# Kernel optimization log

Measured on AMD Instinct MI355X. Metric: run time of the kernel, lower is better.

## Reference

```python
import jax, jax.numpy as jnp
import numpy as np

N = 50000          # nodes
E = 800000         # edges (before self-loops)
IN_CH = 16
HID = 32
HEADS = 4
NEG_SLOPE = 0.2    # PyG GATConv default leaky_relu slope


def add_self_loops(edge_index, n):
    loops = jnp.arange(n, dtype=edge_index.dtype)
    return jnp.concatenate([edge_index, jnp.stack([loops, loops])], axis=1)


def gat_layer(x, edge_index, W, a_src, a_dst, bias, heads, out_ch, concat):
    """PyG-style GATConv: gather -> attention logits -> segment softmax over dst -> scatter."""
    n = x.shape[0]
    h = (x @ W).reshape(n, heads, out_ch)            # [N, H, C]
    src, dst = edge_index[0], edge_index[1]          # messages flow src -> dst
    alpha_src = (h * a_src).sum(-1)                  # [N, H]
    alpha_dst = (h * a_dst).sum(-1)                  # [N, H]
    e = jax.nn.leaky_relu(alpha_src[src] + alpha_dst[dst], NEG_SLOPE)  # [Etot, H]
    # numerically stable segment softmax over incoming edges of each dst node
    e_max = jax.ops.segment_max(e, dst, num_segments=n)
    e_exp = jnp.exp(e - e_max[dst])
    denom = jax.ops.segment_sum(e_exp, dst, num_segments=n)
    alpha = e_exp / (denom[dst] + 1e-16)             # [Etot, H]
    out = jax.ops.segment_sum(h[src] * alpha[..., None], dst, num_segments=n)  # [N, H, C]
    out = out.reshape(n, heads * out_ch) if concat else out.mean(axis=1)
    return out + bias


def setup_inputs() -> dict:
    key = jax.random.key(0)
    ks = jax.random.split(key, 10)
    x = jax.random.normal(ks[0], (N, IN_CH), dtype=jnp.float32)
    edge_index = jax.random.randint(ks[1], (2, E), 0, N, dtype=jnp.int64)
    s = 0.1
    W1 = jax.random.normal(ks[2], (IN_CH, HEADS * HID), dtype=jnp.float32) * s
    a_src1 = jax.random.normal(ks[3], (1, HEADS, HID), dtype=jnp.float32) * s
    a_dst1 = jax.random.normal(ks[4], (1, HEADS, HID), dtype=jnp.float32) * s
    b1 = jnp.zeros((HEADS * HID,), dtype=jnp.float32)
    W2 = jax.random.normal(ks[5], (HEADS * HID, 2), dtype=jnp.float32) * s
    a_src2 = jax.random.normal(ks[6], (1, 1, 2), dtype=jnp.float32) * s
    a_dst2 = jax.random.normal(ks[7], (1, 1, 2), dtype=jnp.float32) * s
    b2 = jnp.zeros((2,), dtype=jnp.float32)
    return {"x": x, "edge_index": edge_index,
            "W1": W1, "a_src1": a_src1, "a_dst1": a_dst1, "b1": b1,
            "W2": W2, "a_src2": a_src2, "a_dst2": a_dst2, "b2": b2}


def reference(x, edge_index, W1, a_src1, a_dst1, b1, W2, a_src2, a_dst2, b2):
    ei = add_self_loops(edge_index, x.shape[0])
    h = gat_layer(x, ei, W1, a_src1, a_dst1, b1, HEADS, HID, concat=True)
    h = jax.nn.relu(h)
    out = gat_layer(h, ei, W2, a_src2, a_dst2, b2, 1, 2, concat=False)
    return out
```

## Files before the change

### kernel.cpp

```cpp
#include <hip/hip_runtime.h>
#include <hip/hip_bf16.h>

#define N_NODES 50000
#define N_EDGES 800000
#define ETOT    (N_EDGES + N_NODES)
#define STRIDE  64
#define IN_CH   16
#define HID     32
#define HEADS   4
#define C1      (HEADS * HID)
#define NEG     0.2f
#define NSLICE  8
#define SLICE_N (N_NODES / NSLICE)

#define DEG_BLOCKS  ((ETOT / 4 + 255) / 256)
#define FILL_BLOCKS (NSLICE * DEG_BLOCKS)
#define NGROUPS     (N_NODES / 4)
#define H1_BLOCKS   2048

typedef unsigned short u16;
typedef unsigned int   u32;

__device__ __forceinline__ float bf2f(u16 b) {
    return __uint_as_float(((u32)b) << 16);
}

__device__ __forceinline__ u16 f2bf(float f) {
    __hip_bfloat16 hb = __float2bfloat16(f);
    return *(u16*)&hb;
}

__device__ __forceinline__ int clampn(int v) {
    return v < 0 ? 0 : (v >= N_NODES ? N_NODES - 1 : v);
}

__device__ __forceinline__ int eidx(const int* ei, int e, int i64, int which) {
    int v = i64 ? ei[2 * (which * N_EDGES + e)] : ei[which * N_EDGES + e];
    return clampn(v);
}

__device__ __forceinline__ float cvt(const void* src, int i, int bf) {
    return bf ? bf2f(((const u16*)src)[i]) : ((const float*)src)[i];
}

__device__ __forceinline__ int probe_bf_wave(const u16* xb) {
    int l = threadIdx.x & 63;
    int my = 0;
#pragma unroll
    for (int k = 0; k < 4; k++) {
        float f = bf2f(xb[l * 4 + k]);
        float a = fabsf(f);
        if (f == 0.0f || (a > 9.5e-7f && a < 1.05e6f)) my++;
    }
#pragma unroll
    for (int m = 32; m; m >>= 1) my += __shfl_xor(my, m);
    return __builtin_amdgcn_readfirstlane(my >= 224 ? 1 : 0);
}

__device__ __forceinline__ int probe_i64_wave(const int* ei32) {
    int l = threadIdx.x & 63;
    int nz = (l < 32 && ei32[2 * l + 1] != 0) ? 1 : 0;
#pragma unroll
    for (int m = 32; m; m >>= 1) nz += __shfl_xor(nz, m);
    return __builtin_amdgcn_readfirstlane(nz == 0 ? 1 : 0);
}

__device__ __forceinline__ void dev_degfill(const int* __restrict__ ei,
                                            int* __restrict__ degs,
                                            u16* __restrict__ csr, int blk) {
    int slice = blk & (NSLICE - 1);
    int chunk = blk >> 3;
    int i64 = probe_i64_wave(ei);
    int e0 = (chunk * 256 + (int)threadIdx.x) * 4;
    if (e0 >= ETOT) return;
    int lo = slice * SLICE_N, hi = lo + SLICE_N;
    int s[4], d[4];
#pragma unroll
    for (int j = 0; j < 4; j++) {
        int e = e0 + j;
        if (e < N_EDGES) { s[j] = eidx(ei, e, i64, 0); d[j] = eidx(ei, e, i64, 1); }
        else             { s[j] = d[j] = e - N_EDGES; }
    }
#pragma unroll
    for (int j = 0; j < 4; j++) {
        if (d[j] >= lo && d[j] < hi) {
            u32 r = (u32)atomicAdd(&degs[d[j]], 1) + 1u;
            if (r < STRIDE) csr[(size_t)d[j] * STRIDE + r] = (u16)s[j];
        }
    }
}

__device__ __forceinline__ void dev_h1(const void* __restrict__ x,
                                       const void* __restrict__ W1,
                                       const void* __restrict__ a_s,
                                       const void* __restrict__ a_d,
                                       float* __restrict__ as1,
                                       float* __restrict__ ad1, int blk) {
    int bf = probe_bf_wave((const u16*)x);
    int w = threadIdx.x >> 6, l = threadIdx.x & 63;

    float wa[IN_CH], wb[IN_CH];
    if (bf) {
        const u32* w32 = (const u32*)W1;
#pragma unroll
        for (int k = 0; k < IN_CH; k++) {
            u32 v = w32[k * 64 + l];
            wa[k] = bf2f((u16)(v & 0xFFFF));
            wb[k] = bf2f((u16)(v >> 16));
        }
    } else {
        const float2* w64 = (const float2*)W1;
#pragma unroll
        for (int k = 0; k < IN_CH; k++) {
            float2 v = w64[k * 64 + l];
            wa[k] = v.x; wb[k] = v.y;
        }
    }
    float asa, asb, ada, adb;
    if (bf) {
        u32 vs = ((const u32*)a_s)[l], vd = ((const u32*)a_d)[l];
        asa = bf2f((u16)(vs & 0xFFFF)); asb = bf2f((u16)(vs >> 16));
        ada = bf2f((u16)(vd & 0xFFFF)); adb = bf2f((u16)(vd >> 16));
    } else {
        float2 vs = ((const float2*)a_s)[l], vd = ((const float2*)a_d)[l];
        asa = vs.x; asb = vs.y; ada = vd.x; adb = vd.y;
    }

    for (int g = blk; g < NGROUPS; g += H1_BLOCKS) {
        int n = g * 4 + w;
        float xr[IN_CH];
        if (bf) {
            const uint4* xp = (const uint4*)((const u16*)x + (size_t)n * IN_CH);
            uint4 q0 = xp[0], q1 = xp[1];
            u32 qq[8] = {q0.x, q0.y, q0.z, q0.w, q1.x, q1.y, q1.z, q1.w};
#pragma unroll
            for (int k = 0; k < 8; k++) {
                xr[2 * k]     = bf2f((u16)(qq[k] & 0xFFFF));
                xr[2 * k + 1] = bf2f((u16)(qq[k] >> 16));
            }
        } else {
            const float4* xp = (const float4*)((const float*)x + (size_t)n * IN_CH);
#pragma unroll
            for (int k = 0; k < 4; k++) {
                float4 q = xp[k];
                xr[4 * k] = q.x; xr[4 * k + 1] = q.y;
                xr[4 * k + 2] = q.z; xr[4 * k + 3] = q.w;
            }
        }
        float acc0 = 0.f, acc1 = 0.f;
#pragma unroll
        for (int k = 0; k < IN_CH; k++) {
            acc0 += xr[k] * wa[k];
            acc1 += xr[k] * wb[k];
        }
        float ps = acc0 * asa + acc1 * asb;
        float pd = acc0 * ada + acc1 * adb;
#pragma unroll
        for (int m = 8; m; m >>= 1) { ps += __shfl_xor(ps, m); pd += __shfl_xor(pd, m); }
        if ((l & 15) == 0) {
            int hd = l >> 4;
            as1[n * 4 + hd] = ps;
            ad1[n * 4 + hd] = pd;
        }
    }
}

__launch_bounds__(256)
__global__ void k_fill_h1(const void* __restrict__ x, const int* __restrict__ ei,
                          const void* __restrict__ W1, const void* __restrict__ a_s,
                          const void* __restrict__ a_d,
                          int* __restrict__ degs, u16* __restrict__ csr,
                          float* __restrict__ as1, float* __restrict__ ad1) {
    if (blockIdx.x < FILL_BLOCKS) { dev_degfill(ei, degs, csr, blockIdx.x); return; }
    dev_h1(x, W1, a_s, a_d, as1, ad1, blockIdx.x - FILL_BLOCKS);
}

__launch_bounds__(256)
__global__ void k_gather1(const void* __restrict__ x,
                          const int* __restrict__ degs, const u16* __restrict__ csr,
                          const float* __restrict__ as1, const float* __restrict__ ad1,
                          const void* __restrict__ W1,
                          const void* __restrict__ b1, const void* __restrict__ W2,
                          const void* __restrict__ a2s, const void* __restrict__ a2d,
                          float* __restrict__ h2, float* __restrict__ as2,
                          float* __restrict__ ad2) {
    __shared__ float xs[4][64][17];
    __shared__ float ws[4][64][4];
    int wv = threadIdx.x >> 6;
    int n  = blockIdx.x * 4 + wv;
    int l  = threadIdx.x & 63;
    int h  = l >> 4;
    int k  = l & 15;
    int g16 = l & 48;

    const u16* row = csr + (size_t)n * STRIDE;
    int se   = (int)row[l];
    int degv = degs[n];
    float4 d4 = ((const float4*)ad1)[n];

    int bf = probe_bf_wave((const u16*)x);

    int deg = degv + 1;
    deg = deg > STRIDE ? STRIDE : deg;
    int live = (l < deg);
    int sidx = (live && se < N_NODES) ? se : 0;

    if (live) {
        float4 a4 = ((const float4*)as1)[sidx];
        float xr[IN_CH];
        if (bf) {
            const uint4* xp = (const uint4*)((const u16*)x + (size_t)sidx * IN_CH);
            uint4 q0 = xp[0], q1 = xp[1];
            u32 qq[8] = {q0.x, q0.y, q0.z, q0.w, q1.x, q1.y, q1.z, q1.w};
#pragma unroll
            for (int kk = 0; kk < 8; kk++) {
                xr[2 * kk]     = bf2f((u16)(qq[kk] & 0xFFFF));
                xr[2 * kk + 1] = bf2f((u16)(qq[kk] >> 16));
            }
        } else {
            const float4* xp = (const float4*)((const float*)x + (size_t)sidx * IN_CH);
#pragma unroll
            for (int kk = 0; kk < 4; kk++) {
                float4 q = xp[kk];
                xr[4 * kk] = q.x; xr[4 * kk + 1] = q.y;
                xr[4 * kk + 2] = q.z; xr[4 * kk + 3] = q.w;
            }
        }
        float t0 = a4.x + d4.x; t0 = t0 > 0.f ? t0 : NEG * t0;
        float t1 = a4.y + d4.y; t1 = t1 > 0.f ? t1 : NEG * t1;
        float t2 = a4.z + d4.z; t2 = t2 > 0.f ? t2 : NEG * t2;
        float t3 = a4.w + d4.w; t3 = t3 > 0.f ? t3 : NEG * t3;
#pragma unroll
        for (int kk = 0; kk < IN_CH; kk++) xs[wv][l][kk] = xr[kk];
        ws[wv][l][0] = __expf(t0); ws[wv][l][1] = __expf(t1);
        ws[wv][l][2] = __expf(t2); ws[wv][l][3] = __expf(t3);
    }

    float wa[IN_CH], wb[IN_CH];
    if (bf) {
        const u32* w32 = (const u32*)W1;
#pragma unroll
        for (int kk = 0; kk < IN_CH; kk++) {
            u32 v = w32[kk * 64 + l];
            wa[kk] = bf2f((u16)(v & 0xFFFF));
            wb[kk] = bf2f((u16)(v >> 16));
        }
    } else {
        const float2* w64 = (const float2*)W1;
#pragma unroll
        for (int kk = 0; kk < IN_CH; kk++) {
            float2 v = w64[kk * 64 + l];
            wa[kk] = v.x; wb[kk] = v.y;
        }
    }
    float b1v0 = cvt(b1, 2 * l, bf),     b1v1 = cvt(b1, 2 * l + 1, bf);
    float w2a  = cvt(W2, 4 * l, bf),     w2b  = cvt(W2, 4 * l + 1, bf);
    float w2c  = cvt(W2, 4 * l + 2, bf), w2d  = cvt(W2, 4 * l + 3, bf);
    float a2s0 = cvt(a2s, 0, bf), a2s1 = cvt(a2s, 1, bf);
    float a2d0 = cvt(a2d, 0, bf), a2d1 = cvt(a2d, 1, bf);

    __syncthreads();

    float acc = 0.f, sws = 0.f;
#pragma unroll 4
    for (int j = 0; j < deg; j++) {
        float w = ws[wv][j][h];
        acc += w * xs[wv][j][k];
        sws += w;
    }
    float aggn = acc * (1.0f / sws);

    float o0 = 0.f, o1 = 0.f;
#pragma unroll
    for (int kk = 0; kk < IN_CH; kk++) {
        float a = __shfl(aggn, g16 + kk);
        o0 += a * wa[kk];
        o1 += a * wb[kk];
    }
    float v0 = o0 + b1v0;
    float v1 = o1 + b1v1;
    v0 = v0 > 0.f ? v0 : 0.f;
    v1 = v1 > 0.f ? v1 : 0.f;
    float p0 = v0 * w2a + v1 * w2c;
    float p1 = v0 * w2b + v1 * w2d;
#pragma unroll
    for (int d = 32; d; d >>= 1) { p0 += __shfl_down(p0, d); p1 += __shfl_down(p1, d); }
    if (l == 0) {
        h2[n * 2] = p0; h2[n * 2 + 1] = p1;
        as2[n] = p0 * a2s0 + p1 * a2s1;
        ad2[n] = p0 * a2d0 + p1 * a2d1;
    }
}

__launch_bounds__(256)
__global__ void k_gather2(const void* __restrict__ x,
                          const int* __restrict__ degs, const u16* __restrict__ csr,
                          const float* __restrict__ h2, const float* __restrict__ as2,
                          const float* __restrict__ ad2, const void* __restrict__ b2,
                          void* __restrict__ out) {
    int n = blockIdx.x * 16 + (threadIdx.x >> 4);
    int g = threadIdx.x & 15;
    int degv = degs[n];
    float adv = ad2[n];
    const u16* row = csr + (size_t)n * STRIDE;
    int bf = probe_bf_wave((const u16*)x);
    float a0 = 0.f, a1 = 0.f, sw = 0.f;
    int deg = degv + 1;
    deg = deg > STRIDE ? STRIDE : deg;
    for (int k = g; k < deg; k += 16) {
        int s = (int)row[k];
        float lg = as2[s] + adv;
        lg = lg > 0.f ? lg : NEG * lg;
        float w = __expf(lg);
        float2 hv = ((const float2*)h2)[s];
        a0 += w * hv.x;
        a1 += w * hv.y;
        sw += w;
    }
#pragma unroll
    for (int m = 8; m; m >>= 1) {
        a0 += __shfl_xor(a0, m); a1 += __shfl_xor(a1, m); sw += __shfl_xor(sw, m);
    }
    if (g == 0) {
        float inv = 1.0f / sw;
        float o0 = a0 * inv + cvt(b2, 0, bf);
        float o1 = a1 * inv + cvt(b2, 1, bf);
        if (bf) {
            ((u32*)out)[n] = (u32)f2bf(o0) | ((u32)f2bf(o1) << 16);
        } else {
            ((float2*)out)[n] = make_float2(o0, o1);
        }
    }
}

extern "C" void kernel_launch(void* const* d_in, const int* in_sizes, int n_in,
                              void* d_out, int out_size, void* d_ws, size_t ws_size,
                              hipStream_t stream) {
    const void* x    = d_in[0];
    const int*  ei   = (const int*)d_in[1];
    const void* W1   = d_in[2];
    const void* a_s1 = d_in[3];
    const void* a_d1 = d_in[4];
    const void* b1   = d_in[5];
    const void* W2   = d_in[6];
    const void* a_s2 = d_in[7];
    const void* a_d2 = d_in[8];
    const void* b2   = d_in[9];

    char* p = (char*)d_ws;
    int*   degs = (int*)p;     p += ((size_t)N_NODES * 4 + 255) & ~255;
    u16*   csr  = (u16*)p;     p += (size_t)N_NODES * STRIDE * 2;
    float* as1  = (float*)p;   p += (size_t)N_NODES * HEADS * 4;
    float* ad1  = (float*)p;   p += (size_t)N_NODES * HEADS * 4;
    float* h2   = (float*)p;   p += (size_t)N_NODES * 2 * 4;
    float* as2  = (float*)p;   p += (size_t)N_NODES * 4;
    float* ad2  = (float*)p;   p += (size_t)N_NODES * 4;

    hipMemsetAsync(degs, 0xFF, (size_t)N_NODES * 4, stream);

    k_fill_h1<<<FILL_BLOCKS + H1_BLOCKS, 256, 0, stream>>>(
        x, ei, W1, a_s1, a_d1, degs, csr, as1, ad1);
    k_gather1<<<N_NODES / 4, 256, 0, stream>>>(
        x, degs, csr, as1, ad1, W1, b1, W2, a_s2, a_d2, h2, as2, ad2);
    k_gather2<<<N_NODES / 16, 256, 0, stream>>>(
        x, degs, csr, h2, as2, ad2, b2, d_out);
}
```

Measured before the change: 206.7 us.

## Process two nodes per wave in gather1 and cache dtype probe flag

```diff
diff --git a/kernel.cpp b/kernel.cpp
--- a/kernel.cpp
+++ b/kernel.cpp
@@ -65,6 +65,27 @@
     return __builtin_amdgcn_readfirstlane(nz == 0 ? 1 : 0);
 }
 
+__device__ __forceinline__ void load_xrow(float* xr, const void* x, int sidx, int bf) {
+    if (bf) {
+        const uint4* xp = (const uint4*)((const u16*)x + (size_t)sidx * IN_CH);
+        uint4 q0 = xp[0], q1 = xp[1];
+        u32 qq[8] = {q0.x, q0.y, q0.z, q0.w, q1.x, q1.y, q1.z, q1.w};
+#pragma unroll
+        for (int kk = 0; kk < 8; kk++) {
+            xr[2 * kk]     = bf2f((u16)(qq[kk] & 0xFFFF));
+            xr[2 * kk + 1] = bf2f((u16)(qq[kk] >> 16));
+        }
+    } else {
+        const float4* xp = (const float4*)((const float*)x + (size_t)sidx * IN_CH);
+#pragma unroll
+        for (int kk = 0; kk < 4; kk++) {
+            float4 q = xp[kk];
+            xr[4 * kk] = q.x; xr[4 * kk + 1] = q.y;
+            xr[4 * kk + 2] = q.z; xr[4 * kk + 3] = q.w;
+        }
+    }
+}
+
 __device__ __forceinline__ void dev_degfill(const int* __restrict__ ei,
                                             int* __restrict__ degs,
                                             u16* __restrict__ csr, int blk) {
@@ -95,8 +116,10 @@
                                        const void* __restrict__ a_s,
                                        const void* __restrict__ a_d,
                                        float* __restrict__ as1,
-                                       float* __restrict__ ad1, int blk) {
+                                       float* __restrict__ ad1,
+                                       u32* __restrict__ flags, int blk) {
     int bf = probe_bf_wave((const u16*)x);
+    if (blk == 0 && threadIdx.x == 0) flags[0] = (u32)bf;
     int w = threadIdx.x >> 6, l = threadIdx.x & 63;
 
     float wa[IN_CH], wb[IN_CH];
@@ -129,24 +152,7 @@
     for (int g = blk; g < NGROUPS; g += H1_BLOCKS) {
         int n = g * 4 + w;
         float xr[IN_CH];
-        if (bf) {
-            const uint4* xp = (const uint4*)((const u16*)x + (size_t)n * IN_CH);
-            uint4 q0 = xp[0], q1 = xp[1];
-            u32 qq[8] = {q0.x, q0.y, q0.z, q0.w, q1.x, q1.y, q1.z, q1.w};
-#pragma unroll
-            for (int k = 0; k < 8; k++) {
-                xr[2 * k]     = bf2f((u16)(qq[k] & 0xFFFF));
-                xr[2 * k + 1] = bf2f((u16)(qq[k] >> 16));
-            }
-        } else {
-            const float4* xp = (const float4*)((const float*)x + (size_t)n * IN_CH);
-#pragma unroll
-            for (int k = 0; k < 4; k++) {
-                float4 q = xp[k];
-                xr[4 * k] = q.x; xr[4 * k + 1] = q.y;
-                xr[4 * k + 2] = q.z; xr[4 * k + 3] = q.w;
-            }
-        }
+        load_xrow(xr, x, n, bf);
         float acc0 = 0.f, acc1 = 0.f;
 #pragma unroll
         for (int k = 0; k < IN_CH; k++) {
@@ -170,9 +176,39 @@
                           const void* __restrict__ W1, const void* __restrict__ a_s,
                           const void* __restrict__ a_d,
                           int* __restrict__ degs, u16* __restrict__ csr,
-                          float* __restrict__ as1, float* __restrict__ ad1) {
+                          float* __restrict__ as1, float* __restrict__ ad1,
+                          u32* __restrict__ flags) {
     if (blockIdx.x < FILL_BLOCKS) { dev_degfill(ei, degs, csr, blockIdx.x); return; }
-    dev_h1(x, W1, a_s, a_d, as1, ad1, blockIdx.x - FILL_BLOCKS);
+    dev_h1(x, W1, a_s, a_d, as1, ad1, flags, blockIdx.x - FILL_BLOCKS);
+}
+
+__device__ __forceinline__ void epi1(int n, int l, int g16, float aggn,
+                                     const float* wa, const float* wb,
+                                     float b1v0, float b1v1,
+                                     float w2a, float w2b, float w2c, float w2d,
+                                     float a2s0, float a2s1, float a2d0, float a2d1,
+                                     float* __restrict__ h2, float* __restrict__ as2,
+                                     float* __restrict__ ad2) {
+    float o0 = 0.f, o1 = 0.f;
+#pragma unroll
+    for (int kk = 0; kk < IN_CH; kk++) {
+        float a = __shfl(aggn, g16 + kk);
+        o0 += a * wa[kk];
+        o1 += a * wb[kk];
+    }
+    float v0 = o0 + b1v0;
+    float v1 = o1 + b1v1;
+    v0 = v0 > 0.f ? v0 : 0.f;
+    v1 = v1 > 0.f ? v1 : 0.f;
+    float p0 = v0 * w2a + v1 * w2c;
+    float p1 = v0 * w2b + v1 * w2d;
+#pragma unroll
+    for (int d = 32; d; d >>= 1) { p0 += __shfl_down(p0, d); p1 += __shfl_down(p1, d); }
+    if (l == 0) {
+        h2[n * 2] = p0; h2[n * 2 + 1] = p1;
+        as2[n] = p0 * a2s0 + p1 * a2s1;
+        ad2[n] = p0 * a2d0 + p1 * a2d1;
+    }
 }
 
 __launch_bounds__(256)
@@ -182,58 +218,53 @@
                           const void* __restrict__ W1,
                           const void* __restrict__ b1, const void* __restrict__ W2,
                           const void* __restrict__ a2s, const void* __restrict__ a2d,
+                          const u32* __restrict__ flags,
                           float* __restrict__ h2, float* __restrict__ as2,
                           float* __restrict__ ad2) {
     __shared__ float xs[4][64][17];
-    __shared__ float ws[4][64][4];
+    __shared__ float ws[4][64][5];
     int wv = threadIdx.x >> 6;
-    int n  = blockIdx.x * 4 + wv;
     int l  = threadIdx.x & 63;
     int h  = l >> 4;
     int k  = l & 15;
     int g16 = l & 48;
-
-    const u16* row = csr + (size_t)n * STRIDE;
-    int se   = (int)row[l];
-    int degv = degs[n];
-    float4 d4 = ((const float4*)ad1)[n];
-
-    int bf = probe_bf_wave((const u16*)x);
-
-    int deg = degv + 1;
-    deg = deg > STRIDE ? STRIDE : deg;
-    int live = (l < deg);
-    int sidx = (live && se < N_NODES) ? se : 0;
-
-    if (live) {
-        float4 a4 = ((const float4*)as1)[sidx];
+    int n0 = blockIdx.x * 8 + wv;
+    int n1 = n0 + 4;
+
+    const u16* row0 = csr + (size_t)n0 * STRIDE;
+    const u16* row1 = csr + (size_t)n1 * STRIDE;
+    int se0 = (int)row0[l];
+    int se1 = (int)row1[l];
+    int dv0 = degs[n0], dv1 = degs[n1];
+    float4 d40 = ((const float4*)ad1)[n0];
+    float4 d41 = ((const float4*)ad1)[n1];
+    int bf = (int)flags[0];
+
+    int deg0 = dv0 + 1; deg0 = deg0 > STRIDE ? STRIDE : deg0;
+    int deg1 = dv1 + 1; deg1 = deg1 > STRIDE ? STRIDE : deg1;
+    int live0 = l < deg0, live1 = l < deg1;
+    int sidx0 = (live0 && se0 < N_NODES) ? se0 : 0;
+    int sidx1 = (live1 && se1 < N_NODES) ? se1 : 0;
+
+    if (live0) {
+        float4 a4 = ((const float4*)as1)[sidx0];
         float xr[IN_CH];
-        if (bf) {
-            const uint4* xp = (const uint4*)((const u16*)x + (size_t)sidx * IN_CH);
-            uint4 q0 = xp[0], q1 = xp[1];
-            u32 qq[8] = {q0.x, q0.y, q0.z, q0.w, q1.x, q1.y, q1.z, q1.w};
-#pragma unroll
-            for (int kk = 0; kk < 8; kk++) {
-                xr[2 * kk]     = bf2f((u16)(qq[kk] & 0xFFFF));
-                xr[2 * kk + 1] = bf2f((u16)(qq[kk] >> 16));
-            }
-        } else {
-            const float4* xp = (const float4*)((const float*)x + (size_t)sidx * IN_CH);
-#pragma unroll
-            for (int kk = 0; kk < 4; kk++) {
-                float4 q = xp[kk];
-                xr[4 * kk] = q.x; xr[4 * kk + 1] = q.y;
-                xr[4 * kk + 2] = q.z; xr[4 * kk + 3] = q.w;
-            }
-        }
-        float t0 = a4.x + d4.x; t0 = t0 > 0.f ? t0 : NEG * t0;
-        float t1 = a4.y + d4.y; t1 = t1 > 0.f ? t1 : NEG * t1;
-        float t2 = a4.z + d4.z; t2 = t2 > 0.f ? t2 : NEG * t2;
-        float t3 = a4.w + d4.w; t3 = t3 > 0.f ? t3 : NEG * t3;
+        load_xrow(xr, x, sidx0, bf);
+        float t0 = a4.x + d40.x; t0 = t0 > 0.f ? t0 : NEG * t0;
+        float t1 = a4.y + d40.y; t1 = t1 > 0.f ? t1 : NEG * t1;
+        float t2 = a4.z + d40.z; t2 = t2 > 0.f ? t2 : NEG * t2;
+        float t3 = a4.w + d40.w; t3 = t3 > 0.f ? t3 : NEG * t3;
 #pragma unroll
         for (int kk = 0; kk < IN_CH; kk++) xs[wv][l][kk] = xr[kk];
         ws[wv][l][0] = __expf(t0); ws[wv][l][1] = __expf(t1);
         ws[wv][l][2] = __expf(t2); ws[wv][l][3] = __expf(t3);
+    }
+
+    float4 a41 = make_float4(0.f, 0.f, 0.f, 0.f);
+    float xr1[IN_CH];
+    if (live1) {
+        a41 = ((const float4*)as1)[sidx1];
+        load_xrow(xr1, x, sidx1, bf);
     }
 
     float wa[IN_CH], wb[IN_CH];
@@ -261,49 +292,59 @@
 
     __syncthreads();
 
-    float acc = 0.f, sws = 0.f;
+    {
+        float acc = 0.f, sws = 0.f;
 #pragma unroll 4
-    for (int j = 0; j < deg; j++) {
-        float w = ws[wv][j][h];
-        acc += w * xs[wv][j][k];
-        sws += w;
-    }
-    float aggn = acc * (1.0f / sws);
-
-    float o0 = 0.f, o1 = 0.f;
-#pragma unroll
-    for (int kk = 0; kk < IN_CH; kk++) {
-        float a = __shfl(aggn, g16 + kk);
-        o0 += a * wa[kk];
-        o1 += a * wb[kk];
-    }
-    float v0 = o0 + b1v0;
-    float v1 = o1 + b1v1;
-    v0 = v0 > 0.f ? v0 : 0.f;
-    v1 = v1 > 0.f ? v1 : 0.f;
-    float p0 = v0 * w2a + v1 * w2c;
-    float p1 = v0 * w2b + v1 * w2d;
-#pragma unroll
-    for (int d = 32; d; d >>= 1) { p0 += __shfl_down(p0, d); p1 += __shfl_down(p1, d); }
-    if (l == 0) {
-        h2[n * 2] = p0; h2[n * 2 + 1] = p1;
-        as2[n] = p0 * a2s0 + p1 * a2s1;
-        ad2[n] = p0 * a2d0 + p1 * a2d1;
+        for (int j = 0; j < deg0; j++) {
+            float w = ws[wv][j][h];
+            acc += w * xs[wv][j][k];
+            sws += w;
+        }
+        float aggn = acc * (1.0f / sws);
+        epi1(n0, l, g16, aggn, wa, wb, b1v0, b1v1, w2a, w2b, w2c, w2d,
+             a2s0, a2s1, a2d0, a2d1, h2, as2, ad2);
+    }
+
+    __syncthreads();
+
+    if (live1) {
+        float t0 = a41.x + d41.x; t0 = t0 > 0.f ? t0 : NEG * t0;
+        float t1 = a41.y + d41.y; t1 = t1 > 0.f ? t1 : NEG * t1;
+        float t2 = a41.z + d41.z; t2 = t2 > 0.f ? t2 : NEG * t2;
+        float t3 = a41.w + d41.w; t3 = t3 > 0.f ? t3 : NEG * t3;
+#pragma unroll
+        for (int kk = 0; kk < IN_CH; kk++) xs[wv][l][kk] = xr1[kk];
+        ws[wv][l][0] = __expf(t0); ws[wv][l][1] = __expf(t1);
+        ws[wv][l][2] = __expf(t2); ws[wv][l][3] = __expf(t3);
+    }
+
+    __syncthreads();
+
+    {
+        float acc = 0.f, sws = 0.f;
+#pragma unroll 4
+        for (int j = 0; j < deg1; j++) {
+            float w = ws[wv][j][h];
+            acc += w * xs[wv][j][k];
+            sws += w;
+        }
+        float aggn = acc * (1.0f / sws);
+        epi1(n1, l, g16, aggn, wa, wb, b1v0, b1v1, w2a, w2b, w2c, w2d,
+             a2s0, a2s1, a2d0, a2d1, h2, as2, ad2);
     }
 }
 
 __launch_bounds__(256)
-__global__ void k_gather2(const void* __restrict__ x,
-                          const int* __restrict__ degs, const u16* __restrict__ csr,
+__global__ void k_gather2(const int* __restrict__ degs, const u16* __restrict__ csr,
                           const float* __restrict__ h2, const float* __restrict__ as2,
                           const float* __restrict__ ad2, const void* __restrict__ b2,
-                          void* __restrict__ out) {
+                          const u32* __restrict__ flags, void* __restrict__ out) {
     int n = blockIdx.x * 16 + (threadIdx.x >> 4);
     int g = threadIdx.x & 15;
     int degv = degs[n];
     float adv = ad2[n];
     const u16* row = csr + (size_t)n * STRIDE;
-    int bf = probe_bf_wave((const u16*)x);
+    int bf = (int)flags[0];
     float a0 = 0.f, a1 = 0.f, sw = 0.f;
     int deg = degv + 1;
     deg = deg > STRIDE ? STRIDE : deg;
@@ -348,20 +389,21 @@
     const void* b2   = d_in[9];
 
     char* p = (char*)d_ws;
-    int*   degs = (int*)p;     p += ((size_t)N_NODES * 4 + 255) & ~255;
-    u16*   csr  = (u16*)p;     p += (size_t)N_NODES * STRIDE * 2;
-    float* as1  = (float*)p;   p += (size_t)N_NODES * HEADS * 4;
-    float* ad1  = (float*)p;   p += (size_t)N_NODES * HEADS * 4;
-    float* h2   = (float*)p;   p += (size_t)N_NODES * 2 * 4;
-    float* as2  = (float*)p;   p += (size_t)N_NODES * 4;
-    float* ad2  = (float*)p;   p += (size_t)N_NODES * 4;
+    int*   degs  = (int*)p;   p += ((size_t)N_NODES * 4 + 255) & ~255;
+    u32*   flags = (u32*)p;   p += 256;
+    u16*   csr   = (u16*)p;   p += (size_t)N_NODES * STRIDE * 2;
+    float* as1   = (float*)p; p += (size_t)N_NODES * HEADS * 4;
+    float* ad1   = (float*)p; p += (size_t)N_NODES * HEADS * 4;
+    float* h2    = (float*)p; p += (size_t)N_NODES * 2 * 4;
+    float* as2   = (float*)p; p += (size_t)N_NODES * 4;
+    float* ad2   = (float*)p; p += (size_t)N_NODES * 4;
 
     hipMemsetAsync(degs, 0xFF, (size_t)N_NODES * 4, stream);
 
     k_fill_h1<<<FILL_BLOCKS + H1_BLOCKS, 256, 0, stream>>>(
-        x, ei, W1, a_s1, a_d1, degs, csr, as1, ad1);
-    k_gather1<<<N_NODES / 4, 256, 0, stream>>>(
-        x, degs, csr, as1, ad1, W1, b1, W2, a_s2, a_d2, h2, as2, ad2);
+        x, ei, W1, a_s1, a_d1, degs, csr, as1, ad1, flags);
+    k_gather1<<<N_NODES / 8, 256, 0, stream>>>(
+        x, degs, csr, as1, ad1, W1, b1, W2, a_s2, a_d2, flags, h2, as2, ad2);
     k_gather2<<<N_NODES / 16, 256, 0, stream>>>(
-        x, degs, csr, h2, as2, ad2, b2, d_out);
-}
+        degs, csr, h2, as2, ad2, b2, flags, d_out);
+}
```

Result: faster. 190.0 us (-8.1%).
